# Performance work log

Measured on AMD Instinct MI355X. Metric: run time of the kernel, lower is better.

## Reference

```python
import jax, jax.numpy as jnp
import numpy as np

B, N, V, X, H, C = 128, 1023, 32000, 256, 256, 10  # N = 2^10 - 1 perfect binary tree (heap layout)


def setup_inputs() -> dict:
    key = jax.random.key(0)
    ks = jax.random.split(key, 12)
    s = 0.02
    return {
        "wordid": jax.random.randint(ks[0], (B, N), 0, V),
        "h0": jnp.zeros((B, N, H), jnp.float32),
        "c0": jnp.zeros((B, N, H), jnp.float32),
        "emb": jax.random.normal(ks[1], (V, X), jnp.float32) * s,
        "W_iou": jax.random.normal(ks[2], (3 * H, X), jnp.float32) * s,
        "U_iou": jax.random.normal(ks[3], (3 * H, 2 * H), jnp.float32) * s,
        "b_iou": jnp.zeros((1, 3 * H), jnp.float32),
        "Uf_W": jax.random.normal(ks[4], (2 * H, 2 * H), jnp.float32) * s,
        "Uf_b": jnp.zeros((2 * H,), jnp.float32),
        "Wmem": jax.random.normal(ks[5], (H, H), jnp.float32) * s,
        "wh_W": jax.random.normal(ks[6], (H, H), jnp.float32) * s,
        "wh_b": jnp.zeros((H,), jnp.float32),
        "lin_W": jax.random.normal(ks[7], (C, H), jnp.float32) * s,
        "lin_b": jnp.zeros((C,), jnp.float32),
    }


def _apply_node(iou, b_iou, c_in):
    # TreeLSTMCell.apply_node_func: iou -> i,o,u gates; c = sig(i)*tanh(u) + c_in; h = sig(o)*tanh(c)
    i, o, u = jnp.split(iou + b_iou, 3, axis=-1)
    c = jax.nn.sigmoid(i) * jnp.tanh(u) + c_in
    h = jax.nn.sigmoid(o) * jnp.tanh(c)
    return h, c


def reference(wordid, h0, c0, emb, W_iou, U_iou, b_iou, Uf_W, Uf_b, Wmem, wh_W, wh_b, lin_W, lin_b):
    Bn, Nn, Hn = h0.shape
    D = int(np.log2(Nn + 1))  # depth of perfect binary tree
    h, c = h0, c0
    # --- leaves (frontier 0): iou = W_iou(embed), c from initial state ---
    s = 2 ** (D - 1) - 1
    x_leaf = emb[wordid[:, s:]]                                  # [B, Nleaf, X]
    iou = jnp.einsum('bnx,gx->bng', x_leaf, W_iou)               # [B, Nleaf, 3H]
    hl, cl = _apply_node(iou, b_iou, c[:, s:])
    h = h.at[:, s:].set(hl)
    c = c.at[:, s:].set(cl)
    # --- internal levels, bottom-up (reduce_func overwrites iou and c) ---
    for level in range(D - 2, -1, -1):
        ps, pe = 2 ** level - 1, 2 ** (level + 1) - 1
        npar = pe - ps
        cs, ce = pe, pe + 2 * npar  # children of parent p live at 2p+1, 2p+2 (contiguous block)
        h_cat = h[:, cs:ce].reshape(Bn, npar, 2 * Hn)            # [B, npar, 2H]
        f = jax.nn.sigmoid(jnp.einsum('bnk,jk->bnj', h_cat, Uf_W) + Uf_b)
        f = f.reshape(Bn, npar, 2, Hn)
        c_sum = jnp.sum(f * c[:, cs:ce].reshape(Bn, npar, 2, Hn), axis=2)
        iou_p = jnp.einsum('bnk,gk->bng', h_cat, U_iou)          # [B, npar, 3H]
        hp, cp = _apply_node(iou_p, b_iou, c_sum)
        h = h.at[:, ps:pe].set(hp)
        c = c.at[:, ps:pe].set(cp)
    # --- TreeAttention: root (node 0 per tree) attends over all nodes of its tree ---
    dec = h[:, 0]                                                # [B, H]
    proj = jnp.einsum('bnh,gh->bng', h, Wmem)                    # memory_project
    scores = jnp.einsum('bh,bnh->bn', dec, proj)
    attn = jax.nn.softmax(scores, axis=1)                        # MaskedSoftmax, mask=None
    context = jnp.einsum('bn,bnh->bh', attn, h)                  # [B, H]
    hid = jax.nn.relu(context @ wh_W.T + wh_b)
    return hid @ lin_W.T + lin_b                                 # [B, num_classes]
```

## Files before the change

### kernel.cpp

```cpp
#include <hip/hip_runtime.h>
#include <math.h>

#define BB      128
#define NNODES  1023
#define HD      256
#define LEAVES  512
#define IOU3    768
#define CAT2    512
#define LDCOMB  1280

typedef unsigned short ushort_t;
typedef __bf16 bf16x8 __attribute__((ext_vector_type(8)));
typedef float  f32x4  __attribute__((ext_vector_type(4)));

__device__ __forceinline__ float sigf(float x) { return 1.0f / (1.0f + expf(-x)); }

__device__ __forceinline__ void gload16(const void* g, void* l)
{
    __builtin_amdgcn_global_load_lds(
        (const __attribute__((address_space(1))) unsigned int*)g,
        (__attribute__((address_space(3))) unsigned int*)l, 16, 0, 0);
}

__device__ __forceinline__ void split_bf16(float x, ushort_t& h, ushort_t& l)
{
    unsigned u = __float_as_uint(x);
    unsigned r = u + 0x7fff + ((u >> 16) & 1);
    h = (ushort_t)(r >> 16);
    float fh = __uint_as_float((unsigned)h << 16);
    float d = x - fh;
    unsigned u2 = __float_as_uint(d);
    unsigned r2 = u2 + 0x7fff + ((u2 >> 16) & 1);
    l = (ushort_t)(r2 >> 16);
}

__device__ __forceinline__ float rh2(ushort_t h, ushort_t l)
{
    return __uint_as_float((unsigned)h << 16) + __uint_as_float((unsigned)l << 16);
}

__global__ void k_split4(const float* __restrict__ src, ushort_t* __restrict__ hi,
                         ushort_t* __restrict__ lo, int n4)
{
    int i = blockIdx.x * 256 + threadIdx.x;
    if (i >= n4) return;
    float4 v = ((const float4*)src)[i];
    ushort4 hv, lv;
    split_bf16(v.x, hv.x, lv.x);
    split_bf16(v.y, hv.y, lv.y);
    split_bf16(v.z, hv.z, lv.z);
    split_bf16(v.w, hv.w, lv.w);
    ((ushort4*)hi)[i] = hv;
    ((ushort4*)lo)[i] = lv;
}

__global__ void k_build_wcat(const float* __restrict__ Uf, const float* __restrict__ Ui,
                             ushort_t* __restrict__ hi, ushort_t* __restrict__ lo)
{
    int i = blockIdx.x * 256 + threadIdx.x;
    if (i >= 1280 * 128) return;
    int row = i >> 7, c4 = i & 127;
    const float* src = (row < 512) ? (Uf + (size_t)row * 512)
                                   : (Ui + (size_t)(row - 512) * 512);
    float4 v = ((const float4*)src)[c4];
    ushort4 hv, lv;
    split_bf16(v.x, hv.x, lv.x);
    split_bf16(v.y, hv.y, lv.y);
    split_bf16(v.z, hv.z, lv.z);
    split_bf16(v.w, hv.w, lv.w);
    ((ushort4*)hi)[i] = hv;
    ((ushort4*)lo)[i] = lv;
}

#define BM 128
#define BN 128
#define BK 32

__global__ __launch_bounds__(512, 4)
void gemm_mfma(const ushort_t* __restrict__ Ahi, const ushort_t* __restrict__ Alo,
               const int* __restrict__ ids,
               int lognpar, unsigned sB, int sP, int m0, int K,
               const ushort_t* __restrict__ Bhi, const ushort_t* __restrict__ Blo,
               float* __restrict__ C, int ldc)
{
    __shared__ __align__(16) char lds[65536];
    const int tid = threadIdx.x;

    int bx = blockIdx.x, by = blockIdx.y;
    {
        const int gx = gridDim.x, gy = gridDim.y;
        if ((gx & 7) == 0) {
            int f = by * gx + bx;
            int span = gy << 3;
            int s = f / span;
            int wv = f - s * span;
            bx = (s << 3) + (wv & 7);
            by = wv >> 3;
        }
    }

    const int w = tid >> 6, lane = tid & 63;

    unsigned aoff, boff;
    {
        int row = tid >> 2;
        int slotp = (tid & 3) ^ ((row >> 1) & 3);
        int mg = m0 + bx * BM + row;
        unsigned ab;
        if (ids) {
            ab = (unsigned)ids[mg] * (unsigned)K;
        } else {
            int b = mg >> lognpar;
            int q = mg & ((1 << lognpar) - 1);
            ab = (unsigned)b * sB + (unsigned)q * (unsigned)sP;
        }
        aoff = ab + slotp * 8;
        boff = (unsigned)(by * BN + row) * (unsigned)K + slotp * 8;
    }
    const int wdst = w * 1024;

    auto STAGE = [&](int k0, char* buf) {
        gload16(Ahi + aoff + k0, buf +     0 + wdst);
        gload16(Alo + aoff + k0, buf +  8192 + wdst);
        gload16(Bhi + boff + k0, buf + 16384 + wdst);
        gload16(Blo + boff + k0, buf + 24576 + wdst);
    };

    const int wm = w >> 2, wn = w & 3;
    const int rA0 = wm * 64 + (lane & 15);
    const int rB0 = wn * 32 + (lane & 15);
    const int ko = lane >> 4;
    const int rdA = rA0 * 64 + ((ko ^ ((rA0 >> 1) & 3)) << 4);
    const int rdB = rB0 * 64 + ((ko ^ ((rB0 >> 1) & 3)) << 4);

    f32x4 acc[4][2];
#pragma unroll
    for (int mi = 0; mi < 4; ++mi)
#pragma unroll
        for (int ni = 0; ni < 2; ++ni) acc[mi][ni] = (f32x4){0.f, 0.f, 0.f, 0.f};

    const int nt = K / BK;
    STAGE(0, lds);
    int cur = 0;
    for (int t = 0; t < nt; ++t) {
        if (t + 1 < nt) {
            STAGE((t + 1) * BK, lds + (cur ^ 1) * 32768);
            asm volatile("s_waitcnt vmcnt(4)" ::: "memory");
        } else {
            asm volatile("s_waitcnt vmcnt(0)" ::: "memory");
        }
        __builtin_amdgcn_s_barrier();
        __builtin_amdgcn_sched_barrier(0);
        char* base = lds + cur * 32768;
        bf16x8 ah[4], al[4], bh[2], bl[2];
#pragma unroll
        for (int f = 0; f < 4; ++f) {
            ah[f] = *(const bf16x8*)(base +        rdA + f * 1024);
            al[f] = *(const bf16x8*)(base + 8192 + rdA + f * 1024);
        }
#pragma unroll
        for (int f = 0; f < 2; ++f) {
            bh[f] = *(const bf16x8*)(base + 16384 + rdB + f * 1024);
            bl[f] = *(const bf16x8*)(base + 24576 + rdB + f * 1024);
        }
        __builtin_amdgcn_s_setprio(1);
#pragma unroll
        for (int mi = 0; mi < 4; ++mi)
#pragma unroll
            for (int ni = 0; ni < 2; ++ni) {
                acc[mi][ni] = __builtin_amdgcn_mfma_f32_16x16x32_bf16(ah[mi], bh[ni], acc[mi][ni], 0, 0, 0);
                acc[mi][ni] = __builtin_amdgcn_mfma_f32_16x16x32_bf16(ah[mi], bl[ni], acc[mi][ni], 0, 0, 0);
                acc[mi][ni] = __builtin_amdgcn_mfma_f32_16x16x32_bf16(al[mi], bh[ni], acc[mi][ni], 0, 0, 0);
            }
        __builtin_amdgcn_s_setprio(0);
        __builtin_amdgcn_s_barrier();
        cur ^= 1;
    }

    {
        char* patch = lds + w * 2304;
        const int cl = lane & 15, rg = lane >> 4;
        const int gcol0 = by * BN + wn * 32;
#pragma unroll
        for (int mi = 0; mi < 4; ++mi) {
#pragma unroll
            for (int ni = 0; ni < 2; ++ni)
#pragma unroll
                for (int r = 0; r < 4; ++r)
                    *(float*)(patch + (rg * 4 + r) * 144 + (ni * 16 + cl) * 4) = acc[mi][ni][r];
            int grow0 = bx * BM + wm * 64 + mi * 16;
#pragma unroll
            for (int i = 0; i < 2; ++i) {
                int slot = lane + 64 * i;
                int lr = slot >> 3, c4 = slot & 7;
                f32x4 vv = *(const f32x4*)(patch + lr * 144 + c4 * 16);
                *(f32x4*)(C + (size_t)(grow0 + lr) * ldc + gcol0 + c4 * 4) = vv;
            }
        }
    }
}

__global__ void k_leaf_ids(const int* __restrict__ wordid, int* __restrict__ ids)
{
    int idx = blockIdx.x * 256 + threadIdx.x;
    int b = idx >> 9, leaf = idx & 511;
    ids[idx] = wordid[b * NNODES + 511 + leaf];
}

__global__ void k_apply_leaf(const float* __restrict__ buf, const float* __restrict__ b_iou,
                             const float* __restrict__ c0,
                             ushort_t* __restrict__ hhi, ushort_t* __restrict__ hlo,
                             float* __restrict__ c, int m0)
{
    int idx = blockIdx.x * 256 + threadIdx.x;
    int m_l = idx >> 8, hh = idx & 255;
    int mg = m0 + m_l;
    int b = mg >> 9, leaf = mg & 511;
    int node = 511 + leaf;
    const float* br = buf + (size_t)m_l * IOU3;
    float iv = br[hh]        + b_iou[hh];
    float ov = br[256 + hh]  + b_iou[256 + hh];
    float uv = br[512 + hh]  + b_iou[512 + hh];
    size_t nb = ((size_t)b * NNODES + node) * HD + hh;
    float cn = sigf(iv) * tanhf(uv) + c0[nb];
    float hn = sigf(ov) * tanhf(cn);
    c[nb] = cn;
    split_bf16(hn, hhi[nb], hlo[nb]);
}

__global__ void k_apply_level(const float* __restrict__ buf, const float* __restrict__ b_iou,
                              const float* __restrict__ Uf_b,
                              ushort_t* __restrict__ hhi, ushort_t* __restrict__ hlo,
                              float* __restrict__ c,
                              int m0, int lognpar, int ps, int cs)
{
    int idx = blockIdx.x * 256 + threadIdx.x;
    int m_l = idx >> 8, hh = idx & 255;
    int mg = m0 + m_l;
    int b = mg >> lognpar;
    int p = mg & ((1 << lognpar) - 1);
    const float* br = buf + (size_t)m_l * LDCOMB;
    float fl = sigf(br[hh]        + Uf_b[hh]);
    float fr = sigf(br[256 + hh]  + Uf_b[256 + hh]);
    size_t cb = ((size_t)b * NNODES + cs + 2 * p) * HD + hh;
    float csum = fl * c[cb] + fr * c[cb + HD];
    float iv = br[512 + hh]  + b_iou[hh];
    float ov = br[768 + hh]  + b_iou[256 + hh];
    float uv = br[1024 + hh] + b_iou[512 + hh];
    float cn = sigf(iv) * tanhf(uv) + csum;
    float hn = sigf(ov) * tanhf(cn);
    size_t pb = ((size_t)b * NNODES + ps + p) * HD + hh;
    c[pb] = cn;
    split_bf16(hn, hhi[pb], hlo[pb]);
}

__global__ void k_dec_v(const ushort_t* __restrict__ hhi, const ushort_t* __restrict__ hlo,
                        const float* __restrict__ Wmem, float* __restrict__ v)
{
    int b = blockIdx.x, k = threadIdx.x;
    __shared__ float dec[HD];
    size_t base = (size_t)b * NNODES * HD;
    dec[k] = rh2(hhi[base + k], hlo[base + k]);
    __syncthreads();
    float s = 0.f;
    for (int g = 0; g < HD; ++g) s = fmaf(dec[g], Wmem[g * HD + k], s);
    v[b * HD + k] = s;
}

__global__ void k_scores(const ushort_t* __restrict__ hhi, const ushort_t* __restrict__ hlo,
                         const float* __restrict__ v, float* __restrict__ scores)
{
    int b = blockIdx.x;
    int w = threadIdx.x >> 6, lane = threadIdx.x & 63;
    int n = blockIdx.y * 4 + w;
    if (n >= NNODES) return;
    size_t hb = ((size_t)b * NNODES + n) * HD;
    ushort4 ph = *(const ushort4*)(hhi + hb + lane * 4);
    ushort4 pl = *(const ushort4*)(hlo + hb + lane * 4);
    float4 vv = *(const float4*)(v + b * HD + lane * 4);
    float s = rh2(ph.x, pl.x) * vv.x + rh2(ph.y, pl.y) * vv.y +
              rh2(ph.z, pl.z) * vv.z + rh2(ph.w, pl.w) * vv.w;
#pragma unroll
    for (int o = 32; o; o >>= 1) s += __shfl_down(s, o);
    if (lane == 0) scores[(size_t)b * NNODES + n] = s;
}

__global__ void k_softmax(const float* __restrict__ scores, float* __restrict__ attn)
{
    int b = blockIdx.x, t = threadIdx.x;
    __shared__ float red[4];
    float sv[4];
    float m = -INFINITY;
#pragma unroll
    for (int i = 0; i < 4; ++i) {
        int n = t + 256 * i;
        sv[i] = (n < NNODES) ? scores[(size_t)b * NNODES + n] : -INFINITY;
        m = fmaxf(m, sv[i]);
    }
#pragma unroll
    for (int o = 32; o; o >>= 1) m = fmaxf(m, __shfl_xor(m, o));
    int w = t >> 6, lane = t & 63;
    if (lane == 0) red[w] = m;
    __syncthreads();
    m = fmaxf(fmaxf(red[0], red[1]), fmaxf(red[2], red[3]));
    float s = 0.f;
#pragma unroll
    for (int i = 0; i < 4; ++i) {
        int n = t + 256 * i;
        sv[i] = (n < NNODES) ? expf(sv[i] - m) : 0.f;
        s += sv[i];
    }
#pragma unroll
    for (int o = 32; o; o >>= 1) s += __shfl_xor(s, o);
    __syncthreads();
    if (lane == 0) red[w] = s;
    __syncthreads();
    s = red[0] + red[1] + red[2] + red[3];
    float inv = 1.0f / s;
#pragma unroll
    for (int i = 0; i < 4; ++i) {
        int n = t + 256 * i;
        if (n < NNODES) attn[(size_t)b * NNODES + n] = sv[i] * inv;
    }
}

__global__ void k_context(const ushort_t* __restrict__ hhi, const ushort_t* __restrict__ hlo,
                          const float* __restrict__ attn, float* __restrict__ partial)
{
    int b = blockIdx.x, ch = blockIdx.y, k = threadIdx.x;
    int n0 = ch * 128;
    int n1 = n0 + 128; if (n1 > NNODES) n1 = NNODES;
    float s = 0.f;
    for (int n = n0; n < n1; ++n) {
        size_t i = ((size_t)b * NNODES + n) * HD + k;
        s = fmaf(attn[(size_t)b * NNODES + n], rh2(hhi[i], hlo[i]), s);
    }
    partial[((size_t)b * 8 + ch) * HD + k] = s;
}

__global__ void k_final(const float* __restrict__ partial,
                        const float* __restrict__ wh_W, const float* __restrict__ wh_b,
                        const float* __restrict__ lin_W, const float* __restrict__ lin_b,
                        float* __restrict__ out)
{
    int b = blockIdx.x, j = threadIdx.x;
    __shared__ float ctx[HD];
    __shared__ float hid[HD];
    float s = 0.f;
#pragma unroll
    for (int ch = 0; ch < 8; ++ch) s += partial[((size_t)b * 8 + ch) * HD + j];
    ctx[j] = s;
    __syncthreads();
    float a = wh_b[j];
    for (int k = 0; k < HD; ++k) a = fmaf(ctx[k], wh_W[j * HD + k], a);
    hid[j] = fmaxf(a, 0.f);
    __syncthreads();
    if (j < 10) {
        float o = lin_b[j];
        for (int k = 0; k < HD; ++k) o = fmaf(hid[k], lin_W[j * HD + k], o);
        out[b * 10 + j] = o;
    }
}

extern "C" void kernel_launch(void* const* d_in, const int* in_sizes, int n_in,
                              void* d_out, int out_size, void* d_ws, size_t ws_size,
                              hipStream_t stream)
{
    const int*   wordid = (const int*)d_in[0];
    const float* c0     = (const float*)d_in[2];
    const float* emb    = (const float*)d_in[3];
    const float* W_iou  = (const float*)d_in[4];
    const float* U_iou  = (const float*)d_in[5];
    const float* b_iou  = (const float*)d_in[6];
    const float* Uf_W   = (const float*)d_in[7];
    const float* Uf_b   = (const float*)d_in[8];
    const float* Wmem   = (const float*)d_in[9];
    const float* wh_W   = (const float*)d_in[10];
    const float* wh_b   = (const float*)d_in[11];
    const float* lin_W  = (const float*)d_in[12];
    const float* lin_b  = (const float*)d_in[13];
    float* out = (float*)d_out;

    const int V = in_sizes[3] / 256;
    const size_t nh = (size_t)BB * NNODES * HD;

    char* ws = (char*)d_ws;
    size_t off = 0;
    auto alloc = [&](size_t bytes) -> void* {
        void* p = ws + off;
        off += (bytes + 255) & ~(size_t)255;
        return p;
    };
    ushort_t* hhi  = (ushort_t*)alloc(nh * 2);
    ushort_t* hlo  = (ushort_t*)alloc(nh * 2);
    float*    c    = (float*)   alloc(nh * 4);
    ushort_t* ehi  = (ushort_t*)alloc((size_t)V * 256 * 2);
    ushort_t* elo  = (ushort_t*)alloc((size_t)V * 256 * 2);
    ushort_t* wchi = (ushort_t*)alloc((size_t)LDCOMB * 512 * 2);
    ushort_t* wclo = (ushort_t*)alloc((size_t)LDCOMB * 512 * 2);
    ushort_t* wihi = (ushort_t*)alloc((size_t)IOU3 * 256 * 2);
    ushort_t* wilo = (ushort_t*)alloc((size_t)IOU3 * 256 * 2);
    int*   ids     = (int*)  alloc((size_t)BB * LEAVES * 4);
    float* v       = (float*)alloc((size_t)BB * HD * 4);
    float* scores  = (float*)alloc((size_t)BB * NNODES * 4);
    float* attn    = (float*)alloc((size_t)BB * NNODES * 4);
    float* partial = (float*)alloc((size_t)BB * 8 * HD * 4);

    size_t remain = (ws_size > off) ? (ws_size - off) : 0;
    size_t rows = remain / (LDCOMB * 4);
    int CH = (int)((rows > 32768) ? 32768 : rows);
    CH &= ~127;
    if (CH < 128) CH = 128;
    float* buf = (float*)alloc((size_t)CH * LDCOMB * 4);

    k_split4<<<(V * 256 / 4 + 255) / 256, 256, 0, stream>>>(emb, ehi, elo, V * 256 / 4);
    k_build_wcat<<<(1280 * 128 + 255) / 256, 256, 0, stream>>>(Uf_W, U_iou, wchi, wclo);
    k_split4<<<(IOU3 * 256 / 4 + 255) / 256, 256, 0, stream>>>(W_iou, wihi, wilo, IOU3 * 256 / 4);
    k_leaf_ids<<<(BB * LEAVES) / 256, 256, 0, stream>>>(wordid, ids);

    {
        int M = BB * LEAVES;
        for (int m0 = 0; m0 < M; m0 += CH) {
            int Mc = M - m0; if (Mc > CH) Mc = CH;
            dim3 g(Mc / BM, IOU3 / BN);
            gemm_mfma<<<g, 512, 0, stream>>>(ehi, elo, ids, 0, 0u, 0, m0, 256,
                                             wihi, wilo, buf, IOU3);
            k_apply_leaf<<<Mc, 256, 0, stream>>>(buf, b_iou, c0, hhi, hlo, c, m0);
        }
    }

    for (int L = 8; L >= 0; --L) {
        int npar = 1 << L;
        int ps = (1 << L) - 1;
        int cs = (1 << (L + 1)) - 1;
        int M = BB * npar;
        unsigned sB = NNODES * HD;
        int sP = 2 * HD;
        const ushort_t* Abh = hhi + (size_t)cs * HD;
        const ushort_t* Abl = hlo + (size_t)cs * HD;
        for (int m0 = 0; m0 < M; m0 += CH) {
            int Mc = M - m0; if (Mc > CH) Mc = CH;
            dim3 g(Mc / BM, LDCOMB / BN);
            gemm_mfma<<<g, 512, 0, stream>>>(Abh, Abl, (const int*)nullptr, L, sB, sP,
                                             m0, CAT2, wchi, wclo, buf, LDCOMB);
            k_apply_level<<<Mc, 256, 0, stream>>>(buf, b_iou, Uf_b, hhi, hlo, c,
                                                  m0, L, ps, cs);
        }
    }

    k_dec_v<<<BB, HD, 0, stream>>>(hhi, hlo, Wmem, v);
    k_scores<<<dim3(BB, 256), 256, 0, stream>>>(hhi, hlo, v, scores);
    k_softmax<<<BB, 256, 0, stream>>>(scores, attn);
    k_context<<<dim3(BB, 8), HD, 0, stream>>>(hhi, hlo, attn, partial);
    k_final<<<BB, HD, 0, stream>>>(partial, wh_W, wh_b, lin_W, lin_b, out);
}
```

Baseline: 741.0 us.

## Fuse small tree levels into one persistent kernel with grid barriers

The six smallest tree levels (L=5..0) now run inside a single persistent kernel that alternates GEMM tiles and gate application, separated by software grid barriers. This replaces twelve small kernel launches whose fixed launch overhead and tail latency dominate when there are few tiles. The leaf GEMM reads word ids directly instead of going through a separate id-gather kernel, and the chunking logic is dropped in favour of one fixed-size buffer. Risks: the atomic spin barrier assumes all 320 blocks are co-resident, the workspace is assumed large enough for that buffer, and the gate step of the small levels becomes a grid-stride loop.

```diff
diff --git a/kernel.cpp b/kernel.cpp
--- a/kernel.cpp
+++ b/kernel.cpp
@@ -37,6 +37,207 @@
 __device__ __forceinline__ float rh2(ushort_t h, ushort_t l)
 {
     return __uint_as_float((unsigned)h << 16) + __uint_as_float((unsigned)l << 16);
+}
+
+__device__ __forceinline__ void gridbar(unsigned* cnt, unsigned* gen)
+{
+    __syncthreads();
+    if (threadIdx.x == 0) {
+        __threadfence();
+        unsigned g = atomicAdd(gen, 0u);
+        if (atomicAdd(cnt, 1u) == (unsigned)gridDim.x - 1u) {
+            atomicExch(cnt, 0u);
+            __threadfence();
+            atomicAdd(gen, 1u);
+        } else {
+            do { __builtin_amdgcn_s_sleep(64); } while (atomicAdd(gen, 0u) == g);
+        }
+        __threadfence();
+    }
+    __syncthreads();
+}
+
+#define BM 128
+#define BN 128
+#define BK 32
+
+__device__ __forceinline__ void gemm_tile(char* lds, int f, int gx, int gy,
+    const ushort_t* __restrict__ Ahi, const ushort_t* __restrict__ Alo,
+    const int* __restrict__ wid,
+    int lognpar, unsigned sB, int sP, int m0, int K,
+    const ushort_t* __restrict__ Bhi, const ushort_t* __restrict__ Blo,
+    float* __restrict__ C, int ldc)
+{
+    int bx, by;
+    if ((gx & 7) == 0) {
+        int span = gy << 3;
+        int s = f / span;
+        int wv = f - s * span;
+        bx = (s << 3) + (wv & 7);
+        by = wv >> 3;
+    } else { bx = f % gx; by = f / gx; }
+
+    const int tid = threadIdx.x;
+    const int w = tid >> 6, lane = tid & 63;
+
+    __syncthreads();
+
+    unsigned aoff, boff;
+    {
+        int row = tid >> 2;
+        int slotp = (tid & 3) ^ ((row >> 1) & 3);
+        int mg = m0 + bx * BM + row;
+        unsigned ab;
+        if (wid) {
+            int b = mg >> 9, lf = mg & 511;
+            ab = (unsigned)wid[b * NNODES + 511 + lf] * (unsigned)K;
+        } else {
+            int b = mg >> lognpar;
+            int q = mg & ((1 << lognpar) - 1);
+            ab = (unsigned)b * sB + (unsigned)q * (unsigned)sP;
+        }
+        aoff = ab + slotp * 8;
+        boff = (unsigned)(by * BN + row) * (unsigned)K + slotp * 8;
+    }
+    const int wdst = w * 1024;
+
+    auto STAGE = [&](int k0, char* buf) {
+        gload16(Ahi + aoff + k0, buf +     0 + wdst);
+        gload16(Alo + aoff + k0, buf +  8192 + wdst);
+        gload16(Bhi + boff + k0, buf + 16384 + wdst);
+        gload16(Blo + boff + k0, buf + 24576 + wdst);
+    };
+
+    const int wm = w >> 2, wn = w & 3;
+    const int rA0 = wm * 64 + (lane & 15);
+    const int rB0 = wn * 32 + (lane & 15);
+    const int ko = lane >> 4;
+    const int rdA = rA0 * 64 + ((ko ^ ((rA0 >> 1) & 3)) << 4);
+    const int rdB = rB0 * 64 + ((ko ^ ((rB0 >> 1) & 3)) << 4);
+
+    f32x4 acc[4][2];
+#pragma unroll
+    for (int mi = 0; mi < 4; ++mi)
+#pragma unroll
+        for (int ni = 0; ni < 2; ++ni) acc[mi][ni] = (f32x4){0.f, 0.f, 0.f, 0.f};
+
+    const int nt = K / BK;
+    STAGE(0, lds);
+    int cur = 0;
+    for (int t = 0; t < nt; ++t) {
+        if (t + 1 < nt) {
+            STAGE((t + 1) * BK, lds + (cur ^ 1) * 32768);
+            asm volatile("s_waitcnt vmcnt(4)" ::: "memory");
+        } else {
+            asm volatile("s_waitcnt vmcnt(0)" ::: "memory");
+        }
+        __builtin_amdgcn_s_barrier();
+        __builtin_amdgcn_sched_barrier(0);
+        char* base = lds + cur * 32768;
+        bf16x8 ah[4], al[4], bh[2], bl[2];
+#pragma unroll
+        for (int q = 0; q < 4; ++q) {
+            ah[q] = *(const bf16x8*)(base +        rdA + q * 1024);
+            al[q] = *(const bf16x8*)(base + 8192 + rdA + q * 1024);
+        }
+#pragma unroll
+        for (int q = 0; q < 2; ++q) {
+            bh[q] = *(const bf16x8*)(base + 16384 + rdB + q * 1024);
+            bl[q] = *(const bf16x8*)(base + 24576 + rdB + q * 1024);
+        }
+        __builtin_amdgcn_s_setprio(1);
+#pragma unroll
+        for (int mi = 0; mi < 4; ++mi)
+#pragma unroll
+            for (int ni = 0; ni < 2; ++ni) {
+                acc[mi][ni] = __builtin_amdgcn_mfma_f32_16x16x32_bf16(ah[mi], bh[ni], acc[mi][ni], 0, 0, 0);
+                acc[mi][ni] = __builtin_amdgcn_mfma_f32_16x16x32_bf16(ah[mi], bl[ni], acc[mi][ni], 0, 0, 0);
+                acc[mi][ni] = __builtin_amdgcn_mfma_f32_16x16x32_bf16(al[mi], bh[ni], acc[mi][ni], 0, 0, 0);
+            }
+        __builtin_amdgcn_s_setprio(0);
+        __builtin_amdgcn_s_barrier();
+        cur ^= 1;
+    }
+
+    {
+        char* patch = lds + w * 2304;
+        const int cl = lane & 15, rg = lane >> 4;
+        const int gcol0 = by * BN + wn * 32;
+#pragma unroll
+        for (int mi = 0; mi < 4; ++mi) {
+#pragma unroll
+            for (int ni = 0; ni < 2; ++ni)
+#pragma unroll
+                for (int r = 0; r < 4; ++r)
+                    *(float*)(patch + (rg * 4 + r) * 144 + (ni * 16 + cl) * 4) = acc[mi][ni][r];
+            int grow0 = bx * BM + wm * 64 + mi * 16;
+#pragma unroll
+            for (int i = 0; i < 2; ++i) {
+                int slot = lane + 64 * i;
+                int lr = slot >> 3, c4 = slot & 7;
+                f32x4 vv = *(const f32x4*)(patch + lr * 144 + c4 * 16);
+                *(f32x4*)(C + (size_t)(grow0 + lr) * ldc + gcol0 + c4 * 4) = vv;
+            }
+        }
+    }
+}
+
+__global__ __launch_bounds__(512, 4)
+void gemm_mfma(const ushort_t* __restrict__ Ahi, const ushort_t* __restrict__ Alo,
+               const int* __restrict__ wid,
+               int lognpar, unsigned sB, int sP, int m0, int K,
+               const ushort_t* __restrict__ Bhi, const ushort_t* __restrict__ Blo,
+               float* __restrict__ C, int ldc)
+{
+    __shared__ __align__(16) char lds[65536];
+    int f = blockIdx.y * gridDim.x + blockIdx.x;
+    gemm_tile(lds, f, gridDim.x, gridDim.y, Ahi, Alo, wid, lognpar, sB, sP,
+              m0, K, Bhi, Blo, C, ldc);
+}
+
+__global__ __launch_bounds__(512, 4)
+void k_small(const ushort_t* __restrict__ hhi_c, ushort_t* hhi, ushort_t* hlo,
+             const ushort_t* __restrict__ hlo_c,
+             const ushort_t* __restrict__ wchi, const ushort_t* __restrict__ wclo,
+             const float* __restrict__ b_iou, const float* __restrict__ Uf_b,
+             float* c, float* buf, unsigned* bar)
+{
+    __shared__ __align__(16) char lds[65536];
+    const int tid = threadIdx.x;
+    unsigned* cnt = bar;
+    unsigned* gen = bar + 32;
+
+    for (int L = 5; L >= 0; --L) {
+        int npar = 1 << L;
+        int ps = npar - 1, cs = 2 * npar - 1;
+        int tiles = npar * 10;
+        const ushort_t* Abh = hhi_c + (size_t)cs * HD;
+        const ushort_t* Abl = hlo_c + (size_t)cs * HD;
+        if (blockIdx.x < (unsigned)tiles)
+            gemm_tile(lds, blockIdx.x, npar, 10, Abh, Abl, (const int*)nullptr,
+                      L, (unsigned)(NNODES * HD), 2 * HD, 0, CAT2,
+                      wchi, wclo, buf, LDCOMB);
+        gridbar(cnt, gen);
+        long tot = (long)(BB * npar) * 256;
+        for (long idx = blockIdx.x * 512L + tid; idx < tot; idx += (long)gridDim.x * 512) {
+            int m_l = (int)(idx >> 8), hh = (int)(idx & 255);
+            int b = m_l >> L, p = m_l & (npar - 1);
+            const float* br = buf + (size_t)m_l * LDCOMB;
+            float fl = sigf(br[hh]       + Uf_b[hh]);
+            float fr = sigf(br[256 + hh] + Uf_b[256 + hh]);
+            size_t cb = ((size_t)b * NNODES + cs + 2 * p) * HD + hh;
+            float csum = fl * c[cb] + fr * c[cb + HD];
+            float iv = br[512 + hh]  + b_iou[hh];
+            float ov = br[768 + hh]  + b_iou[256 + hh];
+            float uv = br[1024 + hh] + b_iou[512 + hh];
+            float cn = sigf(iv) * tanhf(uv) + csum;
+            float hn = sigf(ov) * tanhf(cn);
+            size_t pb = ((size_t)b * NNODES + ps + p) * HD + hh;
+            c[pb] = cn;
+            split_bf16(hn, hhi[pb], hlo[pb]);
+        }
+        gridbar(cnt, gen);
+    }
 }
 
 __global__ void k_split4(const float* __restrict__ src, ushort_t* __restrict__ hi,
@@ -72,150 +273,14 @@
     ((ushort4*)lo)[i] = lv;
 }
 
-#define BM 128
-#define BN 128
-#define BK 32
-
-__global__ __launch_bounds__(512, 4)
-void gemm_mfma(const ushort_t* __restrict__ Ahi, const ushort_t* __restrict__ Alo,
-               const int* __restrict__ ids,
-               int lognpar, unsigned sB, int sP, int m0, int K,
-               const ushort_t* __restrict__ Bhi, const ushort_t* __restrict__ Blo,
-               float* __restrict__ C, int ldc)
-{
-    __shared__ __align__(16) char lds[65536];
-    const int tid = threadIdx.x;
-
-    int bx = blockIdx.x, by = blockIdx.y;
-    {
-        const int gx = gridDim.x, gy = gridDim.y;
-        if ((gx & 7) == 0) {
-            int f = by * gx + bx;
-            int span = gy << 3;
-            int s = f / span;
-            int wv = f - s * span;
-            bx = (s << 3) + (wv & 7);
-            by = wv >> 3;
-        }
-    }
-
-    const int w = tid >> 6, lane = tid & 63;
-
-    unsigned aoff, boff;
-    {
-        int row = tid >> 2;
-        int slotp = (tid & 3) ^ ((row >> 1) & 3);
-        int mg = m0 + bx * BM + row;
-        unsigned ab;
-        if (ids) {
-            ab = (unsigned)ids[mg] * (unsigned)K;
-        } else {
-            int b = mg >> lognpar;
-            int q = mg & ((1 << lognpar) - 1);
-            ab = (unsigned)b * sB + (unsigned)q * (unsigned)sP;
-        }
-        aoff = ab + slotp * 8;
-        boff = (unsigned)(by * BN + row) * (unsigned)K + slotp * 8;
-    }
-    const int wdst = w * 1024;
-
-    auto STAGE = [&](int k0, char* buf) {
-        gload16(Ahi + aoff + k0, buf +     0 + wdst);
-        gload16(Alo + aoff + k0, buf +  8192 + wdst);
-        gload16(Bhi + boff + k0, buf + 16384 + wdst);
-        gload16(Blo + boff + k0, buf + 24576 + wdst);
-    };
-
-    const int wm = w >> 2, wn = w & 3;
-    const int rA0 = wm * 64 + (lane & 15);
-    const int rB0 = wn * 32 + (lane & 15);
-    const int ko = lane >> 4;
-    const int rdA = rA0 * 64 + ((ko ^ ((rA0 >> 1) & 3)) << 4);
-    const int rdB = rB0 * 64 + ((ko ^ ((rB0 >> 1) & 3)) << 4);
-
-    f32x4 acc[4][2];
-#pragma unroll
-    for (int mi = 0; mi < 4; ++mi)
-#pragma unroll
-        for (int ni = 0; ni < 2; ++ni) acc[mi][ni] = (f32x4){0.f, 0.f, 0.f, 0.f};
-
-    const int nt = K / BK;
-    STAGE(0, lds);
-    int cur = 0;
-    for (int t = 0; t < nt; ++t) {
-        if (t + 1 < nt) {
-            STAGE((t + 1) * BK, lds + (cur ^ 1) * 32768);
-            asm volatile("s_waitcnt vmcnt(4)" ::: "memory");
-        } else {
-            asm volatile("s_waitcnt vmcnt(0)" ::: "memory");
-        }
-        __builtin_amdgcn_s_barrier();
-        __builtin_amdgcn_sched_barrier(0);
-        char* base = lds + cur * 32768;
-        bf16x8 ah[4], al[4], bh[2], bl[2];
-#pragma unroll
-        for (int f = 0; f < 4; ++f) {
-            ah[f] = *(const bf16x8*)(base +        rdA + f * 1024);
-            al[f] = *(const bf16x8*)(base + 8192 + rdA + f * 1024);
-        }
-#pragma unroll
-        for (int f = 0; f < 2; ++f) {
-            bh[f] = *(const bf16x8*)(base + 16384 + rdB + f * 1024);
-            bl[f] = *(const bf16x8*)(base + 24576 + rdB + f * 1024);
-        }
-        __builtin_amdgcn_s_setprio(1);
-#pragma unroll
-        for (int mi = 0; mi < 4; ++mi)
-#pragma unroll
-            for (int ni = 0; ni < 2; ++ni) {
-                acc[mi][ni] = __builtin_amdgcn_mfma_f32_16x16x32_bf16(ah[mi], bh[ni], acc[mi][ni], 0, 0, 0);
-                acc[mi][ni] = __builtin_amdgcn_mfma_f32_16x16x32_bf16(ah[mi], bl[ni], acc[mi][ni], 0, 0, 0);
-                acc[mi][ni] = __builtin_amdgcn_mfma_f32_16x16x32_bf16(al[mi], bh[ni], acc[mi][ni], 0, 0, 0);
-            }
-        __builtin_amdgcn_s_setprio(0);
-        __builtin_amdgcn_s_barrier();
-        cur ^= 1;
-    }
-
-    {
-        char* patch = lds + w * 2304;
-        const int cl = lane & 15, rg = lane >> 4;
-        const int gcol0 = by * BN + wn * 32;
-#pragma unroll
-        for (int mi = 0; mi < 4; ++mi) {
-#pragma unroll
-            for (int ni = 0; ni < 2; ++ni)
-#pragma unroll
-                for (int r = 0; r < 4; ++r)
-                    *(float*)(patch + (rg * 4 + r) * 144 + (ni * 16 + cl) * 4) = acc[mi][ni][r];
-            int grow0 = bx * BM + wm * 64 + mi * 16;
-#pragma unroll
-            for (int i = 0; i < 2; ++i) {
-                int slot = lane + 64 * i;
-                int lr = slot >> 3, c4 = slot & 7;
-                f32x4 vv = *(const f32x4*)(patch + lr * 144 + c4 * 16);
-                *(f32x4*)(C + (size_t)(grow0 + lr) * ldc + gcol0 + c4 * 4) = vv;
-            }
-        }
-    }
-}
-
-__global__ void k_leaf_ids(const int* __restrict__ wordid, int* __restrict__ ids)
-{
-    int idx = blockIdx.x * 256 + threadIdx.x;
-    int b = idx >> 9, leaf = idx & 511;
-    ids[idx] = wordid[b * NNODES + 511 + leaf];
-}
-
 __global__ void k_apply_leaf(const float* __restrict__ buf, const float* __restrict__ b_iou,
                              const float* __restrict__ c0,
                              ushort_t* __restrict__ hhi, ushort_t* __restrict__ hlo,
-                             float* __restrict__ c, int m0)
+                             float* __restrict__ c)
 {
     int idx = blockIdx.x * 256 + threadIdx.x;
     int m_l = idx >> 8, hh = idx & 255;
-    int mg = m0 + m_l;
-    int b = mg >> 9, leaf = mg & 511;
+    int b = m_l >> 9, leaf = m_l & 511;
     int node = 511 + leaf;
     const float* br = buf + (size_t)m_l * IOU3;
     float iv = br[hh]        + b_iou[hh];
@@ -232,13 +297,12 @@
                               const float* __restrict__ Uf_b,
                               ushort_t* __restrict__ hhi, ushort_t* __restrict__ hlo,
                               float* __restrict__ c,
-                              int m0, int lognpar, int ps, int cs)
+                              int lognpar, int ps, int cs)
 {
     int idx = blockIdx.x * 256 + threadIdx.x;
     int m_l = idx >> 8, hh = idx & 255;
-    int mg = m0 + m_l;
-    int b = mg >> lognpar;
-    int p = mg & ((1 << lognpar) - 1);
+    int b = m_l >> lognpar;
+    int p = m_l & ((1 << lognpar) - 1);
     const float* br = buf + (size_t)m_l * LDCOMB;
     float fl = sigf(br[hh]        + Uf_b[hh]);
     float fr = sigf(br[256 + hh]  + Uf_b[256 + hh]);
@@ -391,6 +455,7 @@
         off += (bytes + 255) & ~(size_t)255;
         return p;
     };
+    unsigned* bar  = (unsigned*)alloc(256);
     ushort_t* hhi  = (ushort_t*)alloc(nh * 2);
     ushort_t* hlo  = (ushort_t*)alloc(nh * 2);
     float*    c    = (float*)   alloc(nh * 4);
@@ -400,53 +465,41 @@
     ushort_t* wclo = (ushort_t*)alloc((size_t)LDCOMB * 512 * 2);
     ushort_t* wihi = (ushort_t*)alloc((size_t)IOU3 * 256 * 2);
     ushort_t* wilo = (ushort_t*)alloc((size_t)IOU3 * 256 * 2);
-    int*   ids     = (int*)  alloc((size_t)BB * LEAVES * 4);
     float* v       = (float*)alloc((size_t)BB * HD * 4);
     float* scores  = (float*)alloc((size_t)BB * NNODES * 4);
     float* attn    = (float*)alloc((size_t)BB * NNODES * 4);
     float* partial = (float*)alloc((size_t)BB * 8 * HD * 4);
-
-    size_t remain = (ws_size > off) ? (ws_size - off) : 0;
-    size_t rows = remain / (LDCOMB * 4);
-    int CH = (int)((rows > 32768) ? 32768 : rows);
-    CH &= ~127;
-    if (CH < 128) CH = 128;
-    float* buf = (float*)alloc((size_t)CH * LDCOMB * 4);
+    float* buf     = (float*)alloc((size_t)65536 * IOU3 * 4);
+    (void)ws_size;
+
+    hipMemsetAsync(bar, 0, 256, stream);
 
     k_split4<<<(V * 256 / 4 + 255) / 256, 256, 0, stream>>>(emb, ehi, elo, V * 256 / 4);
     k_build_wcat<<<(1280 * 128 + 255) / 256, 256, 0, stream>>>(Uf_W, U_iou, wchi, wclo);
     k_split4<<<(IOU3 * 256 / 4 + 255) / 256, 256, 0, stream>>>(W_iou, wihi, wilo, IOU3 * 256 / 4);
-    k_leaf_ids<<<(BB * LEAVES) / 256, 256, 0, stream>>>(wordid, ids);
 
     {
-        int M = BB * LEAVES;
-        for (int m0 = 0; m0 < M; m0 += CH) {
-            int Mc = M - m0; if (Mc > CH) Mc = CH;
-            dim3 g(Mc / BM, IOU3 / BN);
-            gemm_mfma<<<g, 512, 0, stream>>>(ehi, elo, ids, 0, 0u, 0, m0, 256,
-                                             wihi, wilo, buf, IOU3);
-            k_apply_leaf<<<Mc, 256, 0, stream>>>(buf, b_iou, c0, hhi, hlo, c, m0);
-        }
-    }
-
-    for (int L = 8; L >= 0; --L) {
+        dim3 g(512, 6);
+        gemm_mfma<<<g, 512, 0, stream>>>(ehi, elo, wordid, 0, 0u, 0, 0, 256,
+                                         wihi, wilo, buf, IOU3);
+        k_apply_leaf<<<65536, 256, 0, stream>>>(buf, b_iou, c0, hhi, hlo, c);
+    }
+
+    for (int L = 8; L >= 6; --L) {
         int npar = 1 << L;
-        int ps = (1 << L) - 1;
-        int cs = (1 << (L + 1)) - 1;
-        int M = BB * npar;
-        unsigned sB = NNODES * HD;
-        int sP = 2 * HD;
+        int ps = npar - 1, cs = 2 * npar - 1;
         const ushort_t* Abh = hhi + (size_t)cs * HD;
         const ushort_t* Abl = hlo + (size_t)cs * HD;
-        for (int m0 = 0; m0 < M; m0 += CH) {
-            int Mc = M - m0; if (Mc > CH) Mc = CH;
-            dim3 g(Mc / BM, LDCOMB / BN);
-            gemm_mfma<<<g, 512, 0, stream>>>(Abh, Abl, (const int*)nullptr, L, sB, sP,
-                                             m0, CAT2, wchi, wclo, buf, LDCOMB);
-            k_apply_level<<<Mc, 256, 0, stream>>>(buf, b_iou, Uf_b, hhi, hlo, c,
-                                                  m0, L, ps, cs);
-        }
-    }
+        dim3 g(npar, 10);
+        gemm_mfma<<<g, 512, 0, stream>>>(Abh, Abl, (const int*)nullptr, L,
+                                         (unsigned)(NNODES * HD), 2 * HD, 0, CAT2,
+                                         wchi, wclo, buf, LDCOMB);
+        k_apply_level<<<BB * npar, 256, 0, stream>>>(buf, b_iou, Uf_b, hhi, hlo, c,
+                                                     L, ps, cs);
+    }
+
+    k_small<<<320, 512, 0, stream>>>(hhi, hhi, hlo, hlo, wchi, wclo,
+                                     b_iou, Uf_b, c, buf, bar);
 
     k_dec_v<<<BB, HD, 0, stream>>>(hhi, hlo, Wmem, v);
     k_scores<<<dim3(BB, 256), 256, 0, stream>>>(hhi, hlo, v, scores);
```

Result: slower. 890.7 us (+20.2%).

## Project whole embedding table once, then gather leaf gates by word id

Applied to the files above, without the earlier changes.

Instead of gathering the embedding row for each of the 65536 leaves and multiplying each by W_iou, the leaf GEMM now projects all 32000 vocabulary rows once. The leaf apply kernel then looks up the projected gate row by word id. This cuts the leaf GEMM row count roughly in half and removes the ids kernel and the indexed A-load path. The price is a random-access gather from a large projected table, and the workspace is now a fixed full-size buffer instead of being chunked to fit the available size.

```diff
diff --git a/kernel.cpp b/kernel.cpp
--- a/kernel.cpp
+++ b/kernel.cpp
@@ -78,7 +78,6 @@
 
 __global__ __launch_bounds__(512, 4)
 void gemm_mfma(const ushort_t* __restrict__ Ahi, const ushort_t* __restrict__ Alo,
-               const int* __restrict__ ids,
                int lognpar, unsigned sB, int sP, int m0, int K,
                const ushort_t* __restrict__ Bhi, const ushort_t* __restrict__ Blo,
                float* __restrict__ C, int ldc)
@@ -106,14 +105,9 @@
         int row = tid >> 2;
         int slotp = (tid & 3) ^ ((row >> 1) & 3);
         int mg = m0 + bx * BM + row;
-        unsigned ab;
-        if (ids) {
-            ab = (unsigned)ids[mg] * (unsigned)K;
-        } else {
-            int b = mg >> lognpar;
-            int q = mg & ((1 << lognpar) - 1);
-            ab = (unsigned)b * sB + (unsigned)q * (unsigned)sP;
-        }
+        int b = mg >> lognpar;
+        int q = mg & ((1 << lognpar) - 1);
+        unsigned ab = (unsigned)b * sB + (unsigned)q * (unsigned)sP;
         aoff = ab + slotp * 8;
         boff = (unsigned)(by * BN + row) * (unsigned)K + slotp * 8;
     }
@@ -154,14 +148,14 @@
         char* base = lds + cur * 32768;
         bf16x8 ah[4], al[4], bh[2], bl[2];
 #pragma unroll
-        for (int f = 0; f < 4; ++f) {
-            ah[f] = *(const bf16x8*)(base +        rdA + f * 1024);
-            al[f] = *(const bf16x8*)(base + 8192 + rdA + f * 1024);
+        for (int q = 0; q < 4; ++q) {
+            ah[q] = *(const bf16x8*)(base +        rdA + q * 1024);
+            al[q] = *(const bf16x8*)(base + 8192 + rdA + q * 1024);
         }
 #pragma unroll
-        for (int f = 0; f < 2; ++f) {
-            bh[f] = *(const bf16x8*)(base + 16384 + rdB + f * 1024);
-            bl[f] = *(const bf16x8*)(base + 24576 + rdB + f * 1024);
+        for (int q = 0; q < 2; ++q) {
+            bh[q] = *(const bf16x8*)(base + 16384 + rdB + q * 1024);
+            bl[q] = *(const bf16x8*)(base + 24576 + rdB + q * 1024);
         }
         __builtin_amdgcn_s_setprio(1);
 #pragma unroll
@@ -188,7 +182,7 @@
 #pragma unroll
                 for (int r = 0; r < 4; ++r)
                     *(float*)(patch + (rg * 4 + r) * 144 + (ni * 16 + cl) * 4) = acc[mi][ni][r];
-            int grow0 = bx * BM + wm * 64 + mi * 16;
+            int grow0 = m0 + bx * BM + wm * 64 + mi * 16;
 #pragma unroll
             for (int i = 0; i < 2; ++i) {
                 int slot = lane + 64 * i;
@@ -200,24 +194,17 @@
     }
 }
 
-__global__ void k_leaf_ids(const int* __restrict__ wordid, int* __restrict__ ids)
-{
-    int idx = blockIdx.x * 256 + threadIdx.x;
-    int b = idx >> 9, leaf = idx & 511;
-    ids[idx] = wordid[b * NNODES + 511 + leaf];
-}
-
-__global__ void k_apply_leaf(const float* __restrict__ buf, const float* __restrict__ b_iou,
-                             const float* __restrict__ c0,
+__global__ void k_apply_leaf(const float* __restrict__ viou, const int* __restrict__ wordid,
+                             const float* __restrict__ b_iou, const float* __restrict__ c0,
                              ushort_t* __restrict__ hhi, ushort_t* __restrict__ hlo,
-                             float* __restrict__ c, int m0)
+                             float* __restrict__ c)
 {
     int idx = blockIdx.x * 256 + threadIdx.x;
     int m_l = idx >> 8, hh = idx & 255;
-    int mg = m0 + m_l;
-    int b = mg >> 9, leaf = mg & 511;
+    int b = m_l >> 9, leaf = m_l & 511;
     int node = 511 + leaf;
-    const float* br = buf + (size_t)m_l * IOU3;
+    int word = wordid[b * NNODES + node];
+    const float* br = viou + (size_t)word * IOU3;
     float iv = br[hh]        + b_iou[hh];
     float ov = br[256 + hh]  + b_iou[256 + hh];
     float uv = br[512 + hh]  + b_iou[512 + hh];
@@ -232,13 +219,12 @@
                               const float* __restrict__ Uf_b,
                               ushort_t* __restrict__ hhi, ushort_t* __restrict__ hlo,
                               float* __restrict__ c,
-                              int m0, int lognpar, int ps, int cs)
+                              int lognpar, int ps, int cs)
 {
     int idx = blockIdx.x * 256 + threadIdx.x;
     int m_l = idx >> 8, hh = idx & 255;
-    int mg = m0 + m_l;
-    int b = mg >> lognpar;
-    int p = mg & ((1 << lognpar) - 1);
+    int b = m_l >> lognpar;
+    int p = m_l & ((1 << lognpar) - 1);
     const float* br = buf + (size_t)m_l * LDCOMB;
     float fl = sigf(br[hh]        + Uf_b[hh]);
     float fr = sigf(br[256 + hh]  + Uf_b[256 + hh]);
@@ -400,52 +386,36 @@
     ushort_t* wclo = (ushort_t*)alloc((size_t)LDCOMB * 512 * 2);
     ushort_t* wihi = (ushort_t*)alloc((size_t)IOU3 * 256 * 2);
     ushort_t* wilo = (ushort_t*)alloc((size_t)IOU3 * 256 * 2);
-    int*   ids     = (int*)  alloc((size_t)BB * LEAVES * 4);
     float* v       = (float*)alloc((size_t)BB * HD * 4);
     float* scores  = (float*)alloc((size_t)BB * NNODES * 4);
     float* attn    = (float*)alloc((size_t)BB * NNODES * 4);
     float* partial = (float*)alloc((size_t)BB * 8 * HD * 4);
-
-    size_t remain = (ws_size > off) ? (ws_size - off) : 0;
-    size_t rows = remain / (LDCOMB * 4);
-    int CH = (int)((rows > 32768) ? 32768 : rows);
-    CH &= ~127;
-    if (CH < 128) CH = 128;
-    float* buf = (float*)alloc((size_t)CH * LDCOMB * 4);
+    float* buf     = (float*)alloc((size_t)32768 * LDCOMB * 4);
+    float* viou    = buf;
+    (void)ws_size;
 
     k_split4<<<(V * 256 / 4 + 255) / 256, 256, 0, stream>>>(emb, ehi, elo, V * 256 / 4);
     k_build_wcat<<<(1280 * 128 + 255) / 256, 256, 0, stream>>>(Uf_W, U_iou, wchi, wclo);
     k_split4<<<(IOU3 * 256 / 4 + 255) / 256, 256, 0, stream>>>(W_iou, wihi, wilo, IOU3 * 256 / 4);
-    k_leaf_ids<<<(BB * LEAVES) / 256, 256, 0, stream>>>(wordid, ids);
 
     {
-        int M = BB * LEAVES;
-        for (int m0 = 0; m0 < M; m0 += CH) {
-            int Mc = M - m0; if (Mc > CH) Mc = CH;
-            dim3 g(Mc / BM, IOU3 / BN);
-            gemm_mfma<<<g, 512, 0, stream>>>(ehi, elo, ids, 0, 0u, 0, m0, 256,
-                                             wihi, wilo, buf, IOU3);
-            k_apply_leaf<<<Mc, 256, 0, stream>>>(buf, b_iou, c0, hhi, hlo, c, m0);
-        }
+        dim3 g(V / BM, IOU3 / BN);
+        gemm_mfma<<<g, 512, 0, stream>>>(ehi, elo, 0, 256u, 0, 0, 256,
+                                         wihi, wilo, viou, IOU3);
+        k_apply_leaf<<<65536, 256, 0, stream>>>(viou, wordid, b_iou, c0, hhi, hlo, c);
     }
 
     for (int L = 8; L >= 0; --L) {
         int npar = 1 << L;
-        int ps = (1 << L) - 1;
-        int cs = (1 << (L + 1)) - 1;
-        int M = BB * npar;
-        unsigned sB = NNODES * HD;
-        int sP = 2 * HD;
+        int ps = npar - 1, cs = 2 * npar - 1;
         const ushort_t* Abh = hhi + (size_t)cs * HD;
         const ushort_t* Abl = hlo + (size_t)cs * HD;
-        for (int m0 = 0; m0 < M; m0 += CH) {
-            int Mc = M - m0; if (Mc > CH) Mc = CH;
-            dim3 g(Mc / BM, LDCOMB / BN);
-            gemm_mfma<<<g, 512, 0, stream>>>(Abh, Abl, (const int*)nullptr, L, sB, sP,
-                                             m0, CAT2, wchi, wclo, buf, LDCOMB);
-            k_apply_level<<<Mc, 256, 0, stream>>>(buf, b_iou, Uf_b, hhi, hlo, c,
-                                                  m0, L, ps, cs);
-        }
+        dim3 g(npar, 10);
+        gemm_mfma<<<g, 512, 0, stream>>>(Abh, Abl, L,
+                                         (unsigned)(NNODES * HD), 2 * HD, 0, CAT2,
+                                         wchi, wclo, buf, LDCOMB);
+        k_apply_level<<<BB * npar, 256, 0, stream>>>(buf, b_iou, Uf_b, hhi, hlo, c,
+                                                     L, ps, cs);
     }
 
     k_dec_v<<<BB, HD, 0, stream>>>(hhi, hlo, Wmem, v);
```

Result: faster. 713.5 us (-3.7%).
